# Kernel tuning notes

Hardware: AMD Instinct MI355X
Metric: run time of the kernel (lower is better)

## Reference

```python
import jax, jax.numpy as jnp
import numpy as np

B, N, E, H = 4, 512, 512, 8   # batch, tokens, embedding_channels (=KV_size_S), num_heads
C = 4 * E                      # KV_size_C
D = E // H                     # head dim
EPS = 1e-5                     # InstanceNorm2d default eps


def _inorm(x, axes):
    # InstanceNorm2d (affine=False): normalize over spatial axes with biased variance
    m = jnp.mean(x, axis=axes, keepdims=True)
    v = jnp.var(x, axis=axes, keepdims=True)
    return (x - m) * jax.lax.rsqrt(v + EPS)


def setup_inputs() -> dict:
    key = jax.random.key(0)
    ks = jax.random.split(key, 24)
    s = 0.02
    inp = {
        'emb1': jax.random.normal(ks[0], (B, N, E), jnp.float32),
        'emb2': jax.random.normal(ks[1], (B, N, E), jnp.float32),
        'emb3': jax.random.normal(ks[2], (B, N, E), jnp.float32),
        'emb4': jax.random.normal(ks[3], (B, N, E), jnp.float32),
        'emb_C': jax.random.normal(ks[4], (B, N, C), jnp.float32),
        'Wq1': jax.random.normal(ks[5], (E, E), jnp.float32) * s,
        'Wq2': jax.random.normal(ks[6], (E, E), jnp.float32) * s,
        'Wq3': jax.random.normal(ks[7], (E, E), jnp.float32) * s,
        'Wq4': jax.random.normal(ks[8], (E, E), jnp.float32) * s,
        'Wk': jax.random.normal(ks[9], (E, E), jnp.float32) * s,
        'Wv': jax.random.normal(ks[10], (E, E), jnp.float32) * s,
        'WqC': jax.random.normal(ks[11], (C, C), jnp.float32) * s,
        'WkC': jax.random.normal(ks[12], (C, C), jnp.float32) * s,
        'WvC': jax.random.normal(ks[13], (C, C), jnp.float32) * s,
        'Wo1': jax.random.normal(ks[14], (E, E), jnp.float32) * s,
        'Wo2': jax.random.normal(ks[15], (E, E), jnp.float32) * s,
        'Wo3': jax.random.normal(ks[16], (E, E), jnp.float32) * s,
        'Wo4': jax.random.normal(ks[17], (E, E), jnp.float32) * s,
    }
    return inp


def _heads(x):
    # [B, N, E] -> [B, H, N, D]
    b, n, _ = x.shape
    return x.reshape(b, n, H, D).transpose(0, 2, 1, 3)


def reference(emb1, emb2, emb3, emb4, emb_C,
              Wq1, Wq2, Wq3, Wq4, Wk, Wv, WqC, WkC, WvC,
              Wo1, Wo2, Wo3, Wo4):
    # ---- channel cross-attention ----
    QC = emb_C @ WqC.T            # [B, N, C]
    KC = emb_C @ WkC.T
    VC = emb_C @ WvC.T
    attn_c = jnp.einsum('bnc,bnd->bcd', QC, KC)        # [B, C, C]
    sim_c = jax.nn.softmax(_inorm(attn_c, (1, 2)), axis=-1)  # psi1 + softmax(dim=3)
    ctx_c = jnp.einsum('bcd,bnd->bcn', sim_c, VC)      # [B, C, N]
    T_hat = ctx_c.transpose(0, 2, 1)                   # [B, N, C]
    # split last dim into 4 chunks of E, concat along tokens -> [B, 4N, E]
    KV_S = jnp.concatenate(jnp.split(T_hat, 4, axis=2), axis=1)

    # ---- spatial multi-head cross-attention, shared K/V ----
    K = _heads(KV_S @ Wk.T)       # [B, H, 4N, D]
    V = _heads(KV_S @ Wv.T)

    outs = []
    for emb, Wq, Wo in ((emb1, Wq1, Wo1), (emb2, Wq2, Wo2),
                        (emb3, Wq3, Wo3), (emb4, Wq4, Wo4)):
        Q = _heads(emb @ Wq.T)                          # [B, H, N, D]
        attn = jnp.einsum('bhnd,bhmd->bhnm', Q, K)      # [B, H, N, 4N]
        sim = jax.nn.softmax(_inorm(attn, (2, 3)), axis=-1)  # psi2 + softmax
        ctx = jnp.einsum('bhnm,bhmd->bhnd', sim, V)     # [B, H, N, D]
        ctx = ctx.transpose(0, 2, 1, 3).reshape(emb.shape[0], emb.shape[1], E)
        outs.append(ctx @ Wo.T)
    return tuple(outs)
```

## Files before the change

kernel.cpp:

```cpp
#include <hip/hip_runtime.h>
#include <hip/hip_bf16.h>
#include <hip/hip_fp16.h>

typedef long long i64;
typedef unsigned int u32;
typedef __attribute__((ext_vector_type(8))) short bf16x8;
typedef __attribute__((ext_vector_type(4))) float f32x4;

#define MFMA_BF16 __builtin_amdgcn_mfma_f32_16x16x32_bf16
#define VMCNT(n)  asm volatile("s_waitcnt vmcnt(" #n ")" ::: "memory")
#define LGKM0     asm volatile("s_waitcnt lgkmcnt(0)" ::: "memory")
#define SBAR      __builtin_amdgcn_s_barrier()
#define SCHED0    __builtin_amdgcn_sched_barrier(0)

__device__ __forceinline__ void glds16(const void* g, void* l){
    __builtin_amdgcn_global_load_lds((const __attribute__((address_space(1))) u32*)g,
                                     (__attribute__((address_space(3))) u32*)l, 16, 0, 0);
}
__device__ __forceinline__ void split1(float x, ushort& h, ushort& l){
    unsigned b = __float_as_uint(x);
    h = (ushort)(b >> 16);
    float hf = __uint_as_float(b & 0xFFFF0000u);
    float lf = x - hf;
    l = (ushort)(__float_as_uint(lf) >> 16);
}
__device__ __forceinline__ float bfpair(ushort h, ushort l){
    return __uint_as_float((u32)h << 16) + __uint_as_float((u32)l << 16);
}
__device__ __forceinline__ bf16x8 fragS(const ushort* P, int row, int g){
    return *(const bf16x8*)&P[row*64 + (((g) ^ (row & 7)) << 3)];
}

struct P4 { const void* p[4]; };
struct I4 { int v[4]; };

struct PSJobs { const float* s[13]; ushort* d[13]; int st[14]; };
__global__ __launch_bounds__(256) void presplit(PSJobs J){
    int bid = blockIdx.x, j = 0;
    while (bid >= J.st[j+1]) ++j;
    i64 base = (i64)(bid - J.st[j])*2048 + threadIdx.x*8;
    i64 loOff = (i64)(J.st[j+1] - J.st[j])*2048;
    const float* sp = J.s[j]; ushort* dp = J.d[j];
    float4 a = *(const float4*)&sp[base];
    float4 b = *(const float4*)&sp[base+4];
    float v[8] = {a.x,a.y,a.z,a.w,b.x,b.y,b.z,b.w};
    ushort h[8], l[8];
    #pragma unroll
    for (int t = 0; t < 8; ++t) split1(v[t], h[t], l[t]);
    *(ushort4*)&dp[base]         = make_ushort4(h[0],h[1],h[2],h[3]);
    *(ushort4*)&dp[base+4]       = make_ushort4(h[4],h[5],h[6],h[7]);
    *(ushort4*)&dp[loOff+base]   = make_ushort4(l[0],l[1],l[2],l[3]);
    *(ushort4*)&dp[loOff+base+4] = make_ushort4(l[4],l[5],l[6],l[7]);
}

template<int TM, int OUT>
__global__ __launch_bounds__(256) void gemm_ps(
    P4 Ap, P4 Bp, P4 Cp, I4 cmode, float* __restrict__ stats,
    int K, int zdiv, int ci, int Y, int X,
    i64 ab2, i64 alda, i64 aLo,
    i64 bb2, i64 bldb, i64 bLo,
    i64 cb2, i64 cld, i64 cLo)
{
    constexpr int CW = (TM == 128) ? 64 : 32;
    constexpr int FJ = CW / 16;
    __shared__ ushort Ah[2][TM*32], Al[2][TM*32];
    __shared__ ushort Bh[2][4096], Bl[2][4096];
    __shared__ float sred[4], qred[4];
    const int q8 = gridDim.x >> 3;
    int wg = (blockIdx.x & 7) * q8 + (blockIdx.x >> 3);
    const int z2i = wg % ci; wg /= ci;
    const int y = wg % Y;    wg /= Y;
    const int x = wg % X;
    const int zo = wg / X;
    const int z = zo*ci + z2i;
    const int z1 = z / zdiv, z2 = z % zdiv;
    const int m0 = y*TM, n0 = x*128;

    const int tid = threadIdx.x, lane = tid & 63, wid = tid >> 6;
    const int wm = (TM == 128) ? (wid >> 1) : 0;
    const int wn = (TM == 128) ? (wid & 1) : wid;
    const int fr = lane & 15, kc = lane >> 4;
    const ushort* Aps = (const ushort*)Ap.p[z1] + (i64)z2*ab2 + (i64)m0*alda;
    const ushort* Bps = (const ushort*)Bp.p[z1] + (i64)z2*bb2 + (i64)n0*bldb;

    auto stageAB = [&](int k0, int pb){
        if constexpr (TM == 128) {
            #pragma unroll
            for (int q = 0; q < 2; ++q) {
                int r  = wid*32 + (lane >> 2) + q*16;
                int gs = (lane & 3) ^ ((r >> 1) & 3);
                const ushort* sa = Aps + (i64)r*alda + k0 + gs*8;
                glds16(sa,       &Ah[pb][(wid*32+q*16)*32]);
                glds16(sa + aLo, &Al[pb][(wid*32+q*16)*32]);
            }
        } else {
            int r  = wid*16 + (lane >> 2);
            int gs = (lane & 3) ^ ((r >> 1) & 3);
            const ushort* sa = Aps + (i64)r*alda + k0 + gs*8;
            glds16(sa,       &Ah[pb][(wid*16)*32]);
            glds16(sa + aLo, &Al[pb][(wid*16)*32]);
        }
        #pragma unroll
        for (int q = 0; q < 2; ++q) {
            int r  = wid*32 + (lane >> 2) + q*16;
            int gs = (lane & 3) ^ ((r >> 1) & 3);
            const ushort* sb = Bps + (i64)r*bldb + k0 + gs*8;
            glds16(sb,       &Bh[pb][(wid*32+q*16)*32]);
            glds16(sb + bLo, &Bl[pb][(wid*32+q*16)*32]);
        }
    };
    auto rd = [&](const ushort* P, int row, int kcc)->bf16x8 {
        return *(const bf16x8*)&P[row*32 + ((kcc ^ ((row >> 1) & 3)) << 3)];
    };

    f32x4 acc[4][FJ];
    #pragma unroll
    for (int i = 0; i < 4; ++i)
        #pragma unroll
        for (int j = 0; j < FJ; ++j) acc[i][j] = (f32x4){0.f,0.f,0.f,0.f};

    const int NT = K >> 5;
    stageAB(0, 0); stageAB(32, 1);

    for (int t = 0; t < NT; ++t) {
        const int cur = t & 1;
        if (t + 1 < NT) {
            if constexpr (TM == 128) { VMCNT(8); } else { VMCNT(6); }
        } else { VMCNT(0); }
        SBAR;
        bf16x8 a_h[4], a_l[4], b_h[FJ], b_l[FJ];
        #pragma unroll
        for (int i = 0; i < 4; ++i) {
            int row = wm*64 + i*16 + fr;
            a_h[i] = rd(Ah[cur], row, kc);
            a_l[i] = rd(Al[cur], row, kc);
        }
        #pragma unroll
        for (int j = 0; j < FJ; ++j) {
            int row = wn*CW + j*16 + fr;
            b_h[j] = rd(Bh[cur], row, kc);
            b_l[j] = rd(Bl[cur], row, kc);
        }
        __builtin_amdgcn_s_setprio(1);
        #pragma unroll
        for (int i = 0; i < 4; ++i)
            #pragma unroll
            for (int j = 0; j < FJ; ++j) {
                acc[i][j] = MFMA_BF16(a_h[i], b_h[j], acc[i][j], 0, 0, 0);
                acc[i][j] = MFMA_BF16(a_h[i], b_l[j], acc[i][j], 0, 0, 0);
                acc[i][j] = MFMA_BF16(a_l[i], b_h[j], acc[i][j], 0, 0, 0);
            }
        __builtin_amdgcn_s_setprio(0);
        LGKM0;
        SBAR;
        SCHED0;
        if (t + 2 < NT) stageAB((t+2) << 5, cur);
    }

    const i64 cbase = (i64)z2*cb2;
    if (OUT == 0) {
        float* C = (float*)Cp.p[z1];
        #pragma unroll
        for (int i = 0; i < 4; ++i)
            #pragma unroll
            for (int j = 0; j < FJ; ++j)
                #pragma unroll
                for (int r = 0; r < 4; ++r) {
                    int m = m0 + wm*64 + i*16 + kc*4 + r;
                    int n = n0 + wn*CW + j*16 + fr;
                    C[cbase + (i64)m*cld + n] = acc[i][j][r];
                }
    } else if (OUT == 1) {
        ushort* C = (ushort*)Cp.p[z1];
        const int cfg = cmode.v[z1];
        const int tr = cfg >> 30;
        const i64 ldv = cfg & 0x3FFFFFFF;
        #pragma unroll
        for (int i = 0; i < 4; ++i)
            #pragma unroll
            for (int j = 0; j < FJ; ++j)
                #pragma unroll
                for (int r = 0; r < 4; ++r) {
                    int m = m0 + wm*64 + i*16 + kc*4 + r;
                    int n = n0 + wn*CW + j*16 + fr;
                    ushort h, l; split1(acc[i][j][r], h, l);
                    i64 off = cbase + (tr ? (i64)n*ldv + m : (i64)m*ldv + n);
                    C[off] = h; C[off + cLo] = l;
                }
    } else if (OUT == 2) {
        __half* C = (__half*)Cp.p[z1];
        float ls = 0.f, lq = 0.f;
        #pragma unroll
        for (int i = 0; i < 4; ++i)
            #pragma unroll
            for (int j = 0; j < FJ; ++j)
                #pragma unroll
                for (int r = 0; r < 4; ++r) {
                    int m = m0 + wm*64 + i*16 + kc*4 + r;
                    int n = n0 + wn*CW + j*16 + fr;
                    float v = acc[i][j][r];
                    ls += v; lq += v*v;
                    C[cbase + (i64)m*cld + n] = __float2half(v);
                }
        #pragma unroll
        for (int off = 32; off; off >>= 1) { ls += __shfl_xor(ls, off); lq += __shfl_xor(lq, off); }
        if (lane == 0) { sred[wid] = ls; qred[wid] = lq; }
        __syncthreads();
        if (tid == 0) {
            atomicAdd(&stats[2*z],   sred[0]+sred[1]+sred[2]+sred[3]);
            atomicAdd(&stats[2*z+1], qred[0]+qred[1]+qred[2]+qred[3]);
        }
    } else {
        ushort* C = (ushort*)Cp.p[z1];
        #pragma unroll
        for (int i = 0; i < 4; ++i)
            #pragma unroll
            for (int j = 0; j < FJ; ++j)
                #pragma unroll
                for (int r = 0; r < 4; ++r) {
                    int m = m0 + wm*64 + i*16 + kc*4 + r;
                    int n = n0 + wn*CW + j*16 + fr;
                    ushort h, l; split1(acc[i][j][r], h, l);
                    i64 off = cbase + ((i64)(m >> 9) << 18) + ((i64)n << 9) + (m & 511);
                    C[off] = h; C[off + cLo] = l;
                }
    }
}

__global__ __launch_bounds__(256) void softmax_rows(
    __half* __restrict__ attn, ushort* __restrict__ lo,
    const float* __restrict__ stats, int rows_per_stat, float inv_count)
{
    const int ROWLEN = 2048;
    const int row = blockIdx.x;
    const int sidx = row / rows_per_stat;
    float sm = stats[2*sidx], sq = stats[2*sidx+1];
    float mean = sm * inv_count;
    float var = fmaxf(sq * inv_count - mean*mean, 0.f);
    float scale = rsqrtf(var + 1e-5f);
    __half* rp = attn + (i64)row * ROWLEN;
    ushort* hp = (ushort*)rp;
    ushort* lp = lo + (i64)row * ROWLEN;
    const int tid = threadIdx.x;
    float v[8]; float mx = -3.4e38f;
    #pragma unroll
    for (int s = 0; s < 8; ++s) { float x = __half2float(rp[tid + s*256]) * scale; v[s] = x; mx = fmaxf(mx, x); }
    #pragma unroll
    for (int off = 32; off; off >>= 1) mx = fmaxf(mx, __shfl_xor(mx, off));
    __shared__ float red[4];
    if ((tid & 63) == 0) red[tid >> 6] = mx;
    __syncthreads();
    mx = fmaxf(fmaxf(red[0], red[1]), fmaxf(red[2], red[3]));
    float ls = 0.f;
    #pragma unroll
    for (int s = 0; s < 8; ++s) { float e = __expf(v[s] - mx); v[s] = e; ls += e; }
    #pragma unroll
    for (int off = 32; off; off >>= 1) ls += __shfl_xor(ls, off);
    __syncthreads();
    if ((tid & 63) == 0) red[tid >> 6] = ls;
    __syncthreads();
    float inv = 1.f / (red[0] + red[1] + red[2] + red[3]);
    #pragma unroll
    for (int s = 0; s < 8; ++s) {
        ushort h, l; split1(v[s] * inv, h, l);
        hp[tid + s*256] = h; lp[tid + s*256] = l;
    }
}

__global__ __launch_bounds__(256) void gram64(
    const ushort* __restrict__ hi, i64 loOff, float* __restrict__ parts,
    i64 bstride, i64 zs2)
{
    __shared__ float T[16][68];
    __shared__ float csred[4][64];
    const int z = blockIdx.x;
    const int tid = threadIdx.x;
    const ushort* base = hi + (i64)(z>>3)*bstride + (i64)blockIdx.z*zs2
                       + (i64)blockIdx.y*256*512 + (z&7)*64;
    float g[4][4] = {{0.f}};
    float cs = 0.f;
    const int sr = tid >> 4, sc = (tid & 15) * 4;
    const int col = tid & 63, qq = tid >> 6;
    for (int grp = 0; grp < 16; ++grp) {
        i64 idx = (i64)(grp*16 + sr)*512 + sc;
        ushort4 hv = *(const ushort4*)&base[idx];
        ushort4 lv = *(const ushort4*)&base[loOff + idx];
        float4 ld;
        ld.x = bfpair(hv.x, lv.x); ld.y = bfpair(hv.y, lv.y);
        ld.z = bfpair(hv.z, lv.z); ld.w = bfpair(hv.w, lv.w);
        __syncthreads();
        *(float4*)&T[sr][sc] = ld;
        __syncthreads();
        #pragma unroll
        for (int rr = 0; rr < 16; ++rr) {
            const float4 a = *(const float4*)&T[rr][sr*4];
            const float4 b = *(const float4*)&T[rr][sc];
            g[0][0]+=a.x*b.x; g[0][1]+=a.x*b.y; g[0][2]+=a.x*b.z; g[0][3]+=a.x*b.w;
            g[1][0]+=a.y*b.x; g[1][1]+=a.y*b.y; g[1][2]+=a.y*b.z; g[1][3]+=a.y*b.w;
            g[2][0]+=a.z*b.x; g[2][1]+=a.z*b.y; g[2][2]+=a.z*b.z; g[2][3]+=a.z*b.w;
            g[3][0]+=a.w*b.x; g[3][1]+=a.w*b.y; g[3][2]+=a.w*b.z; g[3][3]+=a.w*b.w;
        }
        cs += T[qq*4+0][col] + T[qq*4+1][col] + T[qq*4+2][col] + T[qq*4+3][col];
    }
    float* outp = parts + (i64)((blockIdx.z*gridDim.y + blockIdx.y)*gridDim.x + blockIdx.x)*4160;
    #pragma unroll
    for (int xx = 0; xx < 4; ++xx)
        #pragma unroll
        for (int yy = 0; yy < 4; ++yy)
            outp[(sr*4+xx)*64 + sc + yy] = g[xx][yy];
    csred[qq][col] = cs;
    __syncthreads();
    if (tid < 64) outp[4096 + tid] = csred[0][tid]+csred[1][tid]+csred[2][tid]+csred[3][tid];
}

__global__ __launch_bounds__(256) void fin_stats(
    const float* __restrict__ gq, const float* __restrict__ gk,
    float* __restrict__ ss)
{
    const int z = blockIdx.x, s = blockIdx.y;
    const int tid = threadIdx.x;
    const int lane = tid & 63, wid = tid >> 6;
    const float* q0 = gq + (i64)((s*2+0)*32 + z)*4160;
    const float* q1 = gq + (i64)((s*2+1)*32 + z)*4160;
    float p2 = 0.f;
    for (int i = tid; i < 4096; i += 256) {
        float a = q0[i] + q1[i];
        float b = 0.f;
        #pragma unroll
        for (int c = 0; c < 8; ++c) b += gk[(i64)(c*32 + z)*4160 + i];
        p2 += a*b;
    }
    float p1 = 0.f;
    if (tid < 64) {
        float a = q0[4096+tid] + q1[4096+tid];
        float b = 0.f;
        #pragma unroll
        for (int c = 0; c < 8; ++c) b += gk[(i64)(c*32 + z)*4160 + 4096 + tid];
        p1 = a*b;
    }
    #pragma unroll
    for (int off = 32; off; off >>= 1) { p2 += __shfl_xor(p2, off); p1 += __shfl_xor(p1, off); }
    __shared__ float r2[4], r1[4];
    if (lane == 0) { r2[wid] = p2; r1[wid] = p1; }
    __syncthreads();
    if (tid == 0) {
        float S2 = r2[0]+r2[1]+r2[2]+r2[3];
        float S1 = r1[0]+r1[1]+r1[2]+r1[3];
        const float inv = 1.f/1048576.f;
        float mu = S1*inv;
        float var = fmaxf(S2*inv - mu*mu, 0.f);
        float sc = rsqrtf(var + 1e-5f);
        ss[(s*32+z)*2] = sc;
        ss[(s*32+z)*2+1] = sc*mu;
    }
}

__global__ __launch_bounds__(256) void flash_ps(
    const ushort* __restrict__ Qp, const ushort* __restrict__ Kp,
    const ushort* __restrict__ Vtp, const float* __restrict__ ss,
    ushort* __restrict__ ctxp)
{
    __shared__ ushort QPh[4096], QPl[4096];
    __shared__ ushort Kh[2][4096], Kl[2][4096];
    __shared__ ushort Vh[2][4096], Vl[2][4096];
    const int q8 = gridDim.x >> 3;
    int wg = (blockIdx.x & 7) * q8 + (blockIdx.x >> 3);
    const int qt = wg & 7, zz = (wg >> 3) & 31, s = wg >> 8;
    const int b = zz >> 3, hD = (zz & 7) * 64;
    const float scale = ss[(s*32+zz)*2], shift = ss[(s*32+zz)*2+1];
    const ushort* Qb = Qp + (i64)s*2097152 + (i64)b*262144 + (i64)(qt*64)*512 + hD;
    const ushort* Kb = Kp + (i64)b*1048576 + hD;
    const ushort* Vb = Vtp + (i64)b*1048576 + (i64)hD*2048;
    const int tid = threadIdx.x, lane = tid & 63, wid = tid >> 6;
    const int wq = wid >> 1, wk = wid & 1, fr = lane & 15, kc = lane >> 4;

    auto stage64 = [&](const ushort* src, i64 ld, i64 lo, ushort* Lh, ushort* Ll){
        #pragma unroll
        for (int q = 0; q < 2; ++q) {
            int rb = wid*16 + q*8;
            int r = rb + (lane >> 3);
            int gs = (lane & 7) ^ (r & 7);
            const ushort* p = src + (i64)r*ld + gs*8;
            glds16(p,      &Lh[rb*64]);
            glds16(p + lo, &Ll[rb*64]);
        }
    };

    stage64(Qb, 512, 1048576, QPh, QPl);
    stage64(Kb, 512, 4194304, Kh[0], Kl[0]);
    stage64(Vb, 2048, 4194304, Vh[0], Vl[0]);
    VMCNT(8); SBAR;
    bf16x8 qh[2][2], ql[2][2];
    #pragma unroll
    for (int i = 0; i < 2; ++i)
        #pragma unroll
        for (int ks = 0; ks < 2; ++ks) {
            int row = wq*32 + i*16 + fr;
            qh[i][ks] = fragS(QPh, row, ks*4 + kc);
            ql[i][ks] = fragS(QPl, row, ks*4 + kc);
        }
    LGKM0; SBAR;
    SCHED0;
    stage64(Kb + (i64)64*512, 512, 4194304, Kh[1], Kl[1]);
    stage64(Vb + 64, 2048, 4194304, Vh[1], Vl[1]);

    f32x4 ctx[2][2];
    #pragma unroll
    for (int i = 0; i < 2; ++i)
        #pragma unroll
        for (int j = 0; j < 2; ++j) ctx[i][j] = (f32x4){0.f,0.f,0.f,0.f};
    float den_lr[2][4] = {{0.f}};

    for (int t = 0; t < 32; ++t) {
        const int cur = t & 1;
        if (t < 31) { VMCNT(8); } else { VMCNT(0); }
        SBAR;
        f32x4 sacc[2][2];
        #pragma unroll
        for (int i = 0; i < 2; ++i)
            #pragma unroll
            for (int j = 0; j < 2; ++j) sacc[i][j] = (f32x4){0.f,0.f,0.f,0.f};
        #pragma unroll
        for (int ks = 0; ks < 2; ++ks) {
            bf16x8 khf[2], klf[2];
            #pragma unroll
            for (int j = 0; j < 2; ++j) {
                int row = wk*32 + j*16 + fr;
                khf[j] = fragS(Kh[cur], row, ks*4 + kc);
                klf[j] = fragS(Kl[cur], row, ks*4 + kc);
            }
            __builtin_amdgcn_s_setprio(1);
            #pragma unroll
            for (int i = 0; i < 2; ++i)
                #pragma unroll
                for (int j = 0; j < 2; ++j) {
                    sacc[i][j] = MFMA_BF16(qh[i][ks], khf[j], sacc[i][j], 0, 0, 0);
                    sacc[i][j] = MFMA_BF16(qh[i][ks], klf[j], sacc[i][j], 0, 0, 0);
                    sacc[i][j] = MFMA_BF16(ql[i][ks], khf[j], sacc[i][j], 0, 0, 0);
                }
            __builtin_amdgcn_s_setprio(0);
        }
        #pragma unroll
        for (int i = 0; i < 2; ++i)
            #pragma unroll
            for (int j = 0; j < 2; ++j)
                #pragma unroll
                for (int r = 0; r < 4; ++r) {
                    float p = __expf(sacc[i][j][r]*scale - shift);
                    den_lr[i][r] += p;
                    ushort h, l; split1(p, h, l);
                    int row = wq*32 + i*16 + kc*4 + r;
                    int col = wk*32 + j*16 + fr;
                    int pos = row*64 + ((((col>>3) ^ (row&7)) << 3) | (col & 7));
                    QPh[pos] = h; QPl[pos] = l;
                }
        LGKM0; SBAR;
        SCHED0;
        if (t < 30) stage64(Kb + (i64)((t+2)*64)*512, 512, 4194304, Kh[cur], Kl[cur]);
        #pragma unroll
        for (int ks = 0; ks < 2; ++ks) {
            bf16x8 vhf[2], vlf[2], pah[2], pal[2];
            #pragma unroll
            for (int j = 0; j < 2; ++j) {
                int row = wk*32 + j*16 + fr;
                vhf[j] = fragS(Vh[cur], row, ks*4 + kc);
                vlf[j] = fragS(Vl[cur], row, ks*4 + kc);
            }
            #pragma unroll
            for (int i = 0; i < 2; ++i) {
                int row = wq*32 + i*16 + fr;
                pah[i] = fragS(QPh, row, ks*4 + kc);
                pal[i] = fragS(QPl, row, ks*4 + kc);
            }
            __builtin_amdgcn_s_setprio(1);
            #pragma unroll
            for (int i = 0; i < 2; ++i)
                #pragma unroll
                for (int j = 0; j < 2; ++j) {
                    ctx[i][j] = MFMA_BF16(pah[i], vhf[j], ctx[i][j], 0, 0, 0);
                    ctx[i][j] = MFMA_BF16(pah[i], vlf[j], ctx[i][j], 0, 0, 0);
                    ctx[i][j] = MFMA_BF16(pal[i], vhf[j], ctx[i][j], 0, 0, 0);
                }
            __builtin_amdgcn_s_setprio(0);
        }
        LGKM0; SBAR;
        SCHED0;
        if (t < 30) stage64(Vb + (t+2)*64, 2048, 4194304, Vh[cur], Vl[cur]);
    }

    float* denf = (float*)QPl;
    #pragma unroll
    for (int i = 0; i < 2; ++i)
        #pragma unroll
        for (int r = 0; r < 4; ++r) {
            float d = den_lr[i][r];
            d += __shfl_xor(d, 1); d += __shfl_xor(d, 2);
            d += __shfl_xor(d, 4); d += __shfl_xor(d, 8);
            if (fr == 0) denf[wk*64 + wq*32 + i*16 + kc*4 + r] = d;
        }
    __syncthreads();
    ushort* Cb = ctxp + (i64)s*2097152 + (i64)b*262144;
    #pragma unroll
    for (int i = 0; i < 2; ++i)
        #pragma unroll
        for (int j = 0; j < 2; ++j)
            #pragma unroll
            for (int r = 0; r < 4; ++r) {
                int row = wq*32 + i*16 + kc*4 + r;
                int col = wk*32 + j*16 + fr;
                float dv = denf[row] + denf[64 + row];
                ushort h, l; split1(ctx[i][j][r] / dv, h, l);
                i64 off = (i64)(qt*64 + row)*512 + hD + col;
                Cb[off] = h; Cb[off + 1048576] = l;
            }
}

static inline P4 p4x(const void* a, const void* b, const void* c, const void* d){
    P4 x; x.p[0]=a; x.p[1]=b; x.p[2]=c; x.p[3]=d; return x;
}
static inline P4 p4x(const void* a){ return p4x(a,a,a,a); }
static inline I4 i4x(int a, int b, int c, int d){ I4 x; x.v[0]=a; x.v[1]=b; x.v[2]=c; x.v[3]=d; return x; }
#define TRC(ld) ((1<<30)|(ld))

extern "C" void kernel_launch(void* const* d_in, const int* in_sizes, int n_in,
                              void* d_out, int out_size, void* d_ws, size_t ws_size,
                              hipStream_t stream)
{
    (void)in_sizes; (void)n_in; (void)out_size;
    const float* emb[4] = {(const float*)d_in[0], (const float*)d_in[1],
                           (const float*)d_in[2], (const float*)d_in[3]};
    const float* embC = (const float*)d_in[4];
    const float* Wq[4] = {(const float*)d_in[5], (const float*)d_in[6],
                          (const float*)d_in[7], (const float*)d_in[8]};
    const float* Wk  = (const float*)d_in[9];
    const float* Wv  = (const float*)d_in[10];
    const float* WqC = (const float*)d_in[11];
    const float* WkC = (const float*)d_in[12];
    const float* WvC = (const float*)d_in[13];
    const float* Wo[4] = {(const float*)d_in[14], (const float*)d_in[15],
                          (const float*)d_in[16], (const float*)d_in[17]};
    float* out = (float*)d_out;

    char* ws = (char*)d_ws;
    const size_t MB = 1024*1024;
    if (ws_size < 128*MB + 512) return;
    auto U = [&](size_t mb){ return (ushort*)(ws + mb*MB); };
    float* stats = (float*)(ws + 122*MB);
    float* ssbuf = (float*)(ws + 122*MB + 1024);
    float* GKp   = (float*)(ws + 48*MB);
    float* GQp   = (float*)(ws + 53*MB);
    __half* scores = (__half*)(ws + 16*MB);

    hipMemsetAsync(stats, 0, 512, stream);

    {
        PSJobs J;
        const float* srcs[13] = {embC, WqC, WkC, WvC, Wk, Wv,
                                 Wq[0],Wq[1],Wq[2],Wq[3], Wo[0],Wo[1],Wo[2]};
        ushort* dsts[13] = {U(0),U(16),U(32),U(48),U(64),U(65),
                            U(66),U(67),U(68),U(69), U(70),U(71),U(72)};
        int blks[13] = {2048,2048,2048,2048,128,128, 128,128,128,128, 128,128,128};
        int a = 0;
        for (int j = 0; j < 13; ++j) { J.s[j]=srcs[j]; J.d[j]=dsts[j]; J.st[j]=a; a+=blks[j]; }
        J.st[13] = a;
        presplit<<<dim3(a), 256, 0, stream>>>(J);
    }
    gemm_ps<64,1><<<dim3(1536), 256, 0, stream>>>(
        p4x(U(0)), p4x(U(16), U(32), U(48), U(48)), p4x(U(74), U(90), U(106), U(106)),
        i4x(TRC(512), TRC(512), 2048, 2048), nullptr,
        2048, 4, 4, 8, 16,
        1048576, 2048, 4194304,   0, 2048, 4194304,   1048576, 0, 4194304);
    {
        PSJobs J;
        const float* srcs[13] = {emb[0], emb[1], emb[2], emb[3], Wo[3],
                                 nullptr,nullptr,nullptr,nullptr,nullptr,nullptr,nullptr,nullptr};
        ushort* dsts[13] = {U(0), U(4), U(8), U(12), U(73),
                            nullptr,nullptr,nullptr,nullptr,nullptr,nullptr,nullptr,nullptr};
        int blks[5] = {512,512,512,512,128};
        int a = 0;
        for (int j = 0; j < 5; ++j) { J.s[j]=srcs[j]; J.d[j]=dsts[j]; J.st[j]=a; a+=blks[j]; }
        for (int j = 5; j < 14; ++j) J.st[j] = a;
        presplit<<<dim3(a), 256, 0, stream>>>(J);
    }
    gemm_ps<128,2><<<dim3(1024), 256, 0, stream>>>(
        p4x(U(74)), p4x(U(90)), p4x(scores), i4x(0,0,0,0), stats,
        512, 4, 1, 16, 16,
        1048576, 512, 4194304,   1048576, 512, 4194304,   4194304, 2048, 0);
    softmax_rows<<<dim3(4*2048), 256, 0, stream>>>(scores, U(74), stats, 2048, 1.f/4194304.f);
    gemm_ps<64,3><<<dim3(512), 256, 0, stream>>>(
        p4x(U(16)), p4x(U(106)), p4x(U(48)), i4x(0,0,0,0), nullptr,
        2048, 4, 1, 32, 4,
        4194304, 2048, 30408704,   1048576, 2048, 4194304,   1048576, 0, 4194304);
    gemm_ps<128,1><<<dim3(512), 256, 0, stream>>>(
        p4x(U(48)), p4x(U(64), U(65), U(65), U(65)), p4x(U(74), U(90), U(90), U(90)),
        i4x(512, TRC(2048), 0, 0), nullptr,
        512, 4, 4, 16, 4,
        1048576, 512, 4194304,   0, 512, 262144,   1048576, 0, 4194304);
    gemm_ps<64,1><<<dim3(512), 256, 0, stream>>>(
        p4x(U(0), U(4), U(8), U(12)), p4x(U(66), U(67), U(68), U(69)),
        p4x(U(106), U(110), U(114), U(118)),
        i4x(512,512,512,512), nullptr,
        512, 4, 4, 8, 4,
        262144, 512, 1048576,   0, 512, 262144,   262144, 0, 1048576);
    gram64<<<dim3(32, 8, 1), 256, 0, stream>>>(U(74), 4194304, GKp, 1048576, 0);
    gram64<<<dim3(32, 2, 4), 256, 0, stream>>>(U(106), 1048576, GQp, 262144, 2097152);
    fin_stats<<<dim3(32, 4), 256, 0, stream>>>(GQp, GKp, ssbuf);
    flash_ps<<<dim3(1024), 256, 0, stream>>>(U(106), U(74), U(90), ssbuf, U(16));
    gemm_ps<64,0><<<dim3(512), 256, 0, stream>>>(
        p4x(U(16), U(20), U(24), U(28)), p4x(U(70), U(71), U(72), U(73)),
        p4x(out, out + 1048576, out + 2097152, out + 3145728),
        i4x(0,0,0,0), nullptr,
        512, 4, 4, 8, 4,
        262144, 512, 1048576,   0, 512, 262144,   262144, 512, 1048576);
}
```

Baseline: 704.6 us.

## Drop XCD block swizzle, transpose flash score MFMA, use 128-row QKV projection tile

Removes the XCD-aware block-index remapping (and its ci parameter) from the GEMM and flash kernels and returns to linear block order. In flash attention the score MFMA now takes K as the A operand and Q as the B operand. That lets each lane write its four P values as one vectorized ushort4 store and reduce the softmax denominator with two cross-lane shuffles instead of four. The QKV projection GEMM switches from 64-row to 128-row tiles with half the grid. The trade-offs are losing L2 locality from the swizzle and having fewer workgroups for the projection.

```diff
diff --git a/kernel.cpp b/kernel.cpp
--- a/kernel.cpp
+++ b/kernel.cpp
@@ -56,7 +56,7 @@
 template<int TM, int OUT>
 __global__ __launch_bounds__(256) void gemm_ps(
     P4 Ap, P4 Bp, P4 Cp, I4 cmode, float* __restrict__ stats,
-    int K, int zdiv, int ci, int Y, int X,
+    int K, int zdiv, int Y, int X,
     i64 ab2, i64 alda, i64 aLo,
     i64 bb2, i64 bldb, i64 bLo,
     i64 cb2, i64 cld, i64 cLo)
@@ -66,13 +66,10 @@
     __shared__ ushort Ah[2][TM*32], Al[2][TM*32];
     __shared__ ushort Bh[2][4096], Bl[2][4096];
     __shared__ float sred[4], qred[4];
-    const int q8 = gridDim.x >> 3;
-    int wg = (blockIdx.x & 7) * q8 + (blockIdx.x >> 3);
-    const int z2i = wg % ci; wg /= ci;
-    const int y = wg % Y;    wg /= Y;
+    int wg = blockIdx.x;
     const int x = wg % X;
-    const int zo = wg / X;
-    const int z = zo*ci + z2i;
+    const int y = (wg / X) % Y;
+    const int z = wg / (X * Y);
     const int z1 = z / zdiv, z2 = z % zdiv;
     const int m0 = y*TM, n0 = x*128;
 
@@ -360,11 +357,10 @@
     const ushort* __restrict__ Vtp, const float* __restrict__ ss,
     ushort* __restrict__ ctxp)
 {
-    __shared__ ushort QPh[4096], QPl[4096];
+    __shared__ ushort Ph[4096], Pl[4096];
     __shared__ ushort Kh[2][4096], Kl[2][4096];
     __shared__ ushort Vh[2][4096], Vl[2][4096];
-    const int q8 = gridDim.x >> 3;
-    int wg = (blockIdx.x & 7) * q8 + (blockIdx.x >> 3);
+    int wg = blockIdx.x;
     const int qt = wg & 7, zz = (wg >> 3) & 31, s = wg >> 8;
     const int b = zz >> 3, hD = (zz & 7) * 64;
     const float scale = ss[(s*32+zz)*2], shift = ss[(s*32+zz)*2+1];
@@ -372,7 +368,9 @@
     const ushort* Kb = Kp + (i64)b*1048576 + hD;
     const ushort* Vb = Vtp + (i64)b*1048576 + (i64)hD*2048;
     const int tid = threadIdx.x, lane = tid & 63, wid = tid >> 6;
-    const int wq = wid >> 1, wk = wid & 1, fr = lane & 15, kc = lane >> 4;
+    const int fr = lane & 15, kc = lane >> 4;
+    const int wkv = wid >> 1, wq2 = wid & 1;
+    const int wq3 = wid >> 1, wd  = wid & 1;
 
     auto stage64 = [&](const ushort* src, i64 ld, i64 lo, ushort* Lh, ushort* Ll){
         #pragma unroll
@@ -386,18 +384,18 @@
         }
     };
 
-    stage64(Qb, 512, 1048576, QPh, QPl);
+    stage64(Qb, 512, 1048576, Ph, Pl);
     stage64(Kb, 512, 4194304, Kh[0], Kl[0]);
     stage64(Vb, 2048, 4194304, Vh[0], Vl[0]);
     VMCNT(8); SBAR;
     bf16x8 qh[2][2], ql[2][2];
     #pragma unroll
-    for (int i = 0; i < 2; ++i)
+    for (int j = 0; j < 2; ++j)
         #pragma unroll
         for (int ks = 0; ks < 2; ++ks) {
-            int row = wq*32 + i*16 + fr;
-            qh[i][ks] = fragS(QPh, row, ks*4 + kc);
-            ql[i][ks] = fragS(QPl, row, ks*4 + kc);
+            int row = wq2*32 + j*16 + fr;
+            qh[j][ks] = fragS(Ph, row, ks*4 + kc);
+            ql[j][ks] = fragS(Pl, row, ks*4 + kc);
         }
     LGKM0; SBAR;
     SCHED0;
@@ -409,7 +407,7 @@
     for (int i = 0; i < 2; ++i)
         #pragma unroll
         for (int j = 0; j < 2; ++j) ctx[i][j] = (f32x4){0.f,0.f,0.f,0.f};
-    float den_lr[2][4] = {{0.f}};
+    float dl[2] = {0.f, 0.f};
 
     for (int t = 0; t < 32; ++t) {
         const int cur = t & 1;
@@ -424,36 +422,39 @@
         for (int ks = 0; ks < 2; ++ks) {
             bf16x8 khf[2], klf[2];
             #pragma unroll
-            for (int j = 0; j < 2; ++j) {
-                int row = wk*32 + j*16 + fr;
-                khf[j] = fragS(Kh[cur], row, ks*4 + kc);
-                klf[j] = fragS(Kl[cur], row, ks*4 + kc);
+            for (int i = 0; i < 2; ++i) {
+                int row = wkv*32 + i*16 + fr;
+                khf[i] = fragS(Kh[cur], row, ks*4 + kc);
+                klf[i] = fragS(Kl[cur], row, ks*4 + kc);
             }
             __builtin_amdgcn_s_setprio(1);
             #pragma unroll
             for (int i = 0; i < 2; ++i)
                 #pragma unroll
                 for (int j = 0; j < 2; ++j) {
-                    sacc[i][j] = MFMA_BF16(qh[i][ks], khf[j], sacc[i][j], 0, 0, 0);
-                    sacc[i][j] = MFMA_BF16(qh[i][ks], klf[j], sacc[i][j], 0, 0, 0);
-                    sacc[i][j] = MFMA_BF16(ql[i][ks], khf[j], sacc[i][j], 0, 0, 0);
+                    sacc[i][j] = MFMA_BF16(khf[i], qh[j][ks], sacc[i][j], 0, 0, 0);
+                    sacc[i][j] = MFMA_BF16(khf[i], ql[j][ks], sacc[i][j], 0, 0, 0);
+                    sacc[i][j] = MFMA_BF16(klf[i], qh[j][ks], sacc[i][j], 0, 0, 0);
                 }
             __builtin_amdgcn_s_setprio(0);
         }
         #pragma unroll
         for (int i = 0; i < 2; ++i)
             #pragma unroll
-            for (int j = 0; j < 2; ++j)
+            for (int j = 0; j < 2; ++j) {
+                ushort h4[4], l4[4];
                 #pragma unroll
                 for (int r = 0; r < 4; ++r) {
                     float p = __expf(sacc[i][j][r]*scale - shift);
-                    den_lr[i][r] += p;
-                    ushort h, l; split1(p, h, l);
-                    int row = wq*32 + i*16 + kc*4 + r;
-                    int col = wk*32 + j*16 + fr;
-                    int pos = row*64 + ((((col>>3) ^ (row&7)) << 3) | (col & 7));
-                    QPh[pos] = h; QPl[pos] = l;
+                    dl[j] += p;
+                    split1(p, h4[r], l4[r]);
                 }
+                int q = wq2*32 + j*16 + fr;
+                int oct = wkv*4 + i*2 + (kc >> 1);
+                int ad = q*64 + ((oct ^ (q & 7)) << 3) + ((kc & 1) << 2);
+                *(ushort4*)&Ph[ad] = make_ushort4(h4[0],h4[1],h4[2],h4[3]);
+                *(ushort4*)&Pl[ad] = make_ushort4(l4[0],l4[1],l4[2],l4[3]);
+            }
         LGKM0; SBAR;
         SCHED0;
         if (t < 30) stage64(Kb + (i64)((t+2)*64)*512, 512, 4194304, Kh[cur], Kl[cur]);
@@ -462,15 +463,16 @@
             bf16x8 vhf[2], vlf[2], pah[2], pal[2];
             #pragma unroll
             for (int j = 0; j < 2; ++j) {
-                int row = wk*32 + j*16 + fr;
+                int row = wd*32 + j*16 + fr;
                 vhf[j] = fragS(Vh[cur], row, ks*4 + kc);
                 vlf[j] = fragS(Vl[cur], row, ks*4 + kc);
             }
             #pragma unroll
             for (int i = 0; i < 2; ++i) {
-                int row = wq*32 + i*16 + fr;
-                pah[i] = fragS(QPh, row, ks*4 + kc);
-                pal[i] = fragS(QPl, row, ks*4 + kc);
+                int q = wq3*32 + i*16 + fr;
+                int o = ks*4 + kc;
+                pah[i] = *(const bf16x8*)&Ph[q*64 + ((o ^ (q & 7)) << 3)];
+                pal[i] = *(const bf16x8*)&Pl[q*64 + ((o ^ (q & 7)) << 3)];
             }
             __builtin_amdgcn_s_setprio(1);
             #pragma unroll
@@ -488,16 +490,13 @@
         if (t < 30) stage64(Vb + (t+2)*64, 2048, 4194304, Vh[cur], Vl[cur]);
     }
 
-    float* denf = (float*)QPl;
-    #pragma unroll
-    for (int i = 0; i < 2; ++i)
-        #pragma unroll
-        for (int r = 0; r < 4; ++r) {
-            float d = den_lr[i][r];
-            d += __shfl_xor(d, 1); d += __shfl_xor(d, 2);
-            d += __shfl_xor(d, 4); d += __shfl_xor(d, 8);
-            if (fr == 0) denf[wk*64 + wq*32 + i*16 + kc*4 + r] = d;
-        }
+    float* denf = (float*)Pl;
+    #pragma unroll
+    for (int j = 0; j < 2; ++j) {
+        float d = dl[j];
+        d += __shfl_xor(d, 16); d += __shfl_xor(d, 32);
+        if (kc == 0) denf[wkv*64 + wq2*32 + j*16 + fr] = d;
+    }
     __syncthreads();
     ushort* Cb = ctxp + (i64)s*2097152 + (i64)b*262144;
     #pragma unroll
@@ -506,8 +505,8 @@
         for (int j = 0; j < 2; ++j)
             #pragma unroll
             for (int r = 0; r < 4; ++r) {
-                int row = wq*32 + i*16 + kc*4 + r;
-                int col = wk*32 + j*16 + fr;
+                int row = wq3*32 + i*16 + kc*4 + r;
+                int col = wd*32 + j*16 + fr;
                 float dv = denf[row] + denf[64 + row];
                 ushort h, l; split1(ctx[i][j][r] / dv, h, l);
                 i64 off = (i64)(qt*64 + row)*512 + hD + col;
@@ -565,10 +564,10 @@
         J.st[13] = a;
         presplit<<<dim3(a), 256, 0, stream>>>(J);
     }
-    gemm_ps<64,1><<<dim3(1536), 256, 0, stream>>>(
+    gemm_ps<128,1><<<dim3(768), 256, 0, stream>>>(
         p4x(U(0)), p4x(U(16), U(32), U(48), U(48)), p4x(U(74), U(90), U(106), U(106)),
         i4x(TRC(512), TRC(512), 2048, 2048), nullptr,
-        2048, 4, 4, 8, 16,
+        2048, 4, 4, 16,
         1048576, 2048, 4194304,   0, 2048, 4194304,   1048576, 0, 4194304);
     {
         PSJobs J;
@@ -584,23 +583,23 @@
     }
     gemm_ps<128,2><<<dim3(1024), 256, 0, stream>>>(
         p4x(U(74)), p4x(U(90)), p4x(scores), i4x(0,0,0,0), stats,
-        512, 4, 1, 16, 16,
+        512, 4, 16, 16,
         1048576, 512, 4194304,   1048576, 512, 4194304,   4194304, 2048, 0);
     softmax_rows<<<dim3(4*2048), 256, 0, stream>>>(scores, U(74), stats, 2048, 1.f/4194304.f);
     gemm_ps<64,3><<<dim3(512), 256, 0, stream>>>(
         p4x(U(16)), p4x(U(106)), p4x(U(48)), i4x(0,0,0,0), nullptr,
-        2048, 4, 1, 32, 4,
+        2048, 4, 32, 4,
         4194304, 2048, 30408704,   1048576, 2048, 4194304,   1048576, 0, 4194304);
     gemm_ps<128,1><<<dim3(512), 256, 0, stream>>>(
         p4x(U(48)), p4x(U(64), U(65), U(65), U(65)), p4x(U(74), U(90), U(90), U(90)),
         i4x(512, TRC(2048), 0, 0), nullptr,
-        512, 4, 4, 16, 4,
+        512, 4, 16, 4,
         1048576, 512, 4194304,   0, 512, 262144,   1048576, 0, 4194304);
     gemm_ps<64,1><<<dim3(512), 256, 0, stream>>>(
         p4x(U(0), U(4), U(8), U(12)), p4x(U(66), U(67), U(68), U(69)),
         p4x(U(106), U(110), U(114), U(118)),
         i4x(512,512,512,512), nullptr,
-        512, 4, 4, 8, 4,
+        512, 4, 8, 4,
         262144, 512, 1048576,   0, 512, 262144,   262144, 0, 1048576);
     gram64<<<dim3(32, 8, 1), 256, 0, stream>>>(U(74), 4194304, GKp, 1048576, 0);
     gram64<<<dim3(32, 2, 4), 256, 0, stream>>>(U(106), 1048576, GQp, 262144, 2097152);
@@ -610,6 +609,6 @@
         p4x(U(16), U(20), U(24), U(28)), p4x(U(70), U(71), U(72), U(73)),
         p4x(out, out + 1048576, out + 2097152, out + 3145728),
         i4x(0,0,0,0), nullptr,
-        512, 4, 4, 8, 4,
+        512, 4, 8, 4,
         262144, 512, 1048576,   0, 512, 262144,   262144, 512, 1048576);
 }
```

After: 661.5 us. 1.07x faster.
